# Optimization experiments

Hardware: AMD Instinct MI355X
Metric: run time of the kernel (lower is better)

The kernel has to match this reference:

```python
import jax, jax.numpy as jnp
import numpy as np

N_NODES = 100000
N_FEAT = 512
N_HID = 64
N_CLASS = 16
N_EDGES = 3200000
K = 10
ALPHA = 0.1


def setup_inputs() -> dict:
    key = jax.random.key(0)
    k1, k2, k3, k4, k5, k6 = jax.random.split(key, 6)
    x = jax.random.normal(k1, (N_NODES, N_FEAT), dtype=jnp.float32)
    edge_index = jax.random.randint(k2, (2, N_EDGES), 0, N_NODES, dtype=jnp.int64)
    # Linear params (torch Linear: y = x @ W.T + b), kaiming-uniform-ish scale
    s1 = 1.0 / np.sqrt(N_FEAT)
    W1 = jax.random.uniform(k3, (N_HID, N_FEAT), jnp.float32, -s1, s1)
    b1 = jax.random.uniform(k4, (N_HID,), jnp.float32, -s1, s1)
    s2 = 1.0 / np.sqrt(N_HID)
    W2 = jax.random.uniform(k5, (N_CLASS, N_HID), jnp.float32, -s2, s2)
    b2 = jax.random.uniform(k6, (N_CLASS,), jnp.float32, -s2, s2)
    return {"x": x, "W1": W1, "b1": b1, "W2": W2, "b2": b2, "edge_index": edge_index}


def _gcn_norm(edge_index, num_nodes):
    # add self-loops
    loops = jnp.arange(num_nodes, dtype=edge_index.dtype)
    row = jnp.concatenate([edge_index[0], loops])
    col = jnp.concatenate([edge_index[1], loops])
    deg = jax.ops.segment_sum(jnp.ones_like(col, dtype=jnp.float32), col,
                              num_segments=num_nodes)
    dis = jnp.where(deg > 0, jax.lax.rsqrt(jnp.maximum(deg, 1.0)), 0.0)
    norm = dis[row] * dis[col]  # symmetric D^-1/2 A D^-1/2
    return row, col, norm


def reference(x, W1, b1, W2, b2, edge_index):
    n = x.shape[0]
    # MLP (eval mode: dropout disabled)
    h = jax.nn.relu(x @ W1.T + b1)
    h0 = h @ W2.T + b2  # [N, nclass]
    # APPNP propagation: x_{k+1} = (1-alpha) * A_hat x_k + alpha * h0
    row, col, norm = _gcn_norm(edge_index, n)

    def step(h_cur, _):
        msg = norm[:, None] * h_cur[row]           # gather source nodes
        agg = jax.ops.segment_sum(msg, col, num_segments=n)  # scatter-add to targets
        return (1.0 - ALPHA) * agg + ALPHA * h0, None

    out, _ = jax.lax.scan(step, h0, None, length=K)
    return jax.nn.log_softmax(out, axis=1)
```

## Files before the change

kernel.cpp:

```cpp
#include <hip/hip_runtime.h>

#define NN 100000
#define NE 3200000
#define NCLS 16
#define NHID 64
#define NFEAT 512

#define NBUCK 391
#define PB 256
#define EPB 12500
#define CNT_TOT (NBUCK * PB)
#define CAP 10240

typedef __bf16 bf8 __attribute__((ext_vector_type(8)));
typedef short s8v __attribute__((ext_vector_type(8)));
typedef float f4 __attribute__((ext_vector_type(4)));
typedef unsigned short us8 __attribute__((ext_vector_type(8)));

union bu { s8v s; bf8 b; };

__device__ __forceinline__ float bf2f(unsigned short u) {
  union { unsigned int i; float f; } c; c.i = ((unsigned int)u) << 16; return c.f;
}
__device__ __forceinline__ unsigned short f2bf(float f) {
  unsigned int i = __float_as_uint(f);
  unsigned int r = (i + 0x7fffu + ((i >> 16) & 1u)) >> 16;
  return (unsigned short)r;
}

__global__ void probe_kernel(const unsigned short* __restrict__ x16,
                             const int* __restrict__ ei,
                             int* __restrict__ flags) {
  if (threadIdx.x == 0) {
    int inr = 0;
    for (int i = 0; i < 256; ++i) {
      float a = fabsf(bf2f(x16[2 * i]));
      if (a > 1e-3f && a < 16.0f) inr++;
    }
    flags[0] = (inr < 128) ? 1 : 0;
    int any = 0;
    for (int i = 0; i < 1024; ++i) any |= ei[2 * i + 1];
    flags[1] = (any != 0) ? 1 : 0;
  }
}

__device__ __forceinline__ int edge_val(const int* ei, int f_i32, long elem) {
  return f_i32 ? ei[elem] : ei[2 * elem];
}

__device__ __forceinline__ float ldf(const void* p, long i, int f32) {
  return f32 ? ((const float*)p)[i] : bf2f(((const unsigned short*)p)[i]);
}

__device__ __forceinline__ bf8 ld8(const void* p, long idx, int f32) {
  bu u;
  if (!f32) {
    u.b = *(const bf8*)((const unsigned short*)p + idx);
  } else {
    const f4* q = (const f4*)((const float*)p + idx);
    f4 a0 = q[0], a1 = q[1];
#pragma unroll
    for (int j = 0; j < 4; ++j) {
      u.s[j] = (short)f2bf(a0[j]);
      u.s[4 + j] = (short)f2bf(a1[j]);
    }
  }
  return u.b;
}

__global__ void sentinel_kernel(float* __restrict__ out, float v) {
  out[blockIdx.x * 256 + threadIdx.x] = v;
}

__global__ __launch_bounds__(256) void hist_kernel(const int* __restrict__ ei,
                                                   const int* __restrict__ flags,
                                                   unsigned int* __restrict__ cnt) {
  __shared__ unsigned int h[NBUCK];
  int tid = threadIdx.x;
  int f_i32 = flags[1];
  for (int i = tid; i < NBUCK; i += 256) h[i] = 0;
  __syncthreads();
  long e0 = (long)blockIdx.x * EPB;
  for (int t = tid; t < EPB; t += 256) {
    int dst = edge_val(ei, f_i32, (long)NE + e0 + t);
    atomicAdd(&h[dst >> 8], 1u);
  }
  __syncthreads();
  for (int i = tid; i < NBUCK; i += 256) cnt[(long)i * PB + blockIdx.x] = h[i];
}

__global__ __launch_bounds__(1024) void scan2_kernel(unsigned int* __restrict__ cnt) {
  __shared__ unsigned int sums[1024];
  const int C = 98;
  int t = threadIdx.x;
  int c0 = t * C;
  int c1 = min(c0 + C, CNT_TOT);
  unsigned int s = 0;
  for (int i = c0; i < c1; ++i) s += cnt[i];
  sums[t] = s;
  __syncthreads();
  for (int d = 1; d < 1024; d <<= 1) {
    unsigned int v = (t >= d) ? sums[t - d] : 0u;
    __syncthreads();
    sums[t] += v;
    __syncthreads();
  }
  unsigned int off = (t == 0) ? 0u : sums[t - 1];
  for (int i = c0; i < c1; ++i) {
    unsigned int v = cnt[i];
    cnt[i] = off;
    off += v;
  }
}

__global__ __launch_bounds__(256) void part_kernel(const int* __restrict__ ei,
                                                   const int* __restrict__ flags,
                                                   const unsigned int* __restrict__ cnt,
                                                   unsigned int* __restrict__ part) {
  __shared__ unsigned int cur[NBUCK];
  int tid = threadIdx.x;
  int b = blockIdx.x;
  int f_i32 = flags[1];
  for (int i = tid; i < NBUCK; i += 256) cur[i] = cnt[(long)i * PB + b];
  __syncthreads();
  long e0 = (long)b * EPB;
  for (int t = tid; t < EPB; t += 256) {
    int dst = edge_val(ei, f_i32, (long)NE + e0 + t);
    int src = edge_val(ei, f_i32, e0 + t);
    unsigned int pos = atomicAdd(&cur[dst >> 8], 1u);
    part[pos] = ((unsigned int)(dst & 255) << 20) | (unsigned int)src;
  }
}

__global__ __launch_bounds__(256) void csrb_kernel(const unsigned int* __restrict__ part,
                                                   const unsigned int* __restrict__ cnt,
                                                   unsigned int* __restrict__ csr,
                                                   unsigned int* __restrict__ deg,
                                                   unsigned int* __restrict__ offs,
                                                   float* __restrict__ dis) {
  __shared__ unsigned int sp[CAP];
  __shared__ unsigned int hcnt[256];
  __shared__ unsigned int hoff[256];
  int tid = threadIdx.x;
  int k = blockIdx.x;
  unsigned int start = cnt[(long)k * PB];
  unsigned int end = (k == NBUCK - 1) ? (unsigned int)NE : cnt[(long)(k + 1) * PB];
  int n = (int)(end - start);

  hcnt[tid] = 0;
  __syncthreads();
  for (int j = tid; j < n; j += 256) {
    unsigned int v = part[start + j];
    if (j < CAP) sp[j] = v;
    atomicAdd(&hcnt[v >> 20], 1u);
  }
  __syncthreads();

  unsigned int myc = hcnt[tid];
  hoff[tid] = myc;
  __syncthreads();
  for (int d = 1; d < 256; d <<= 1) {
    unsigned int v = (tid >= d) ? hoff[tid - d] : 0u;
    __syncthreads();
    hoff[tid] += v;
    __syncthreads();
  }
  unsigned int excl = hoff[tid] - myc;

  int node = k * 256 + tid;
  if (node < NN) {
    deg[node] = myc;
    offs[node] = start + excl;
    dis[node] = rsqrtf((float)(myc + 1u));
  }
  __syncthreads();
  hcnt[tid] = excl;
  __syncthreads();
  for (int j = tid; j < n; j += 256) {
    unsigned int v = (j < CAP) ? sp[j] : part[start + j];
    unsigned int pos = atomicAdd(&hcnt[v >> 20], 1u);
    csr[start + pos] = v & 0xFFFFFu;
  }
}

__global__ __launch_bounds__(256) void mlp_kernel(const void* __restrict__ xv,
                                                  const void* __restrict__ W1v,
                                                  const void* __restrict__ b1v,
                                                  const void* __restrict__ W2v,
                                                  const void* __restrict__ b2v,
                                                  const int* __restrict__ flags,
                                                  unsigned short* __restrict__ h0) {
  __shared__ float hl[64][65];
  __shared__ float w2l[16][65];
  __shared__ float b2l[16];

  int f32 = flags[0];
  int tid = threadIdx.x;
  int wave = tid >> 6;
  int lane = tid & 63;
  int quad = lane >> 4;
  int l16 = lane & 15;
  long rowBase = (long)blockIdx.x * 64;
  long mrow = rowBase + wave * 16 + l16;
  long mC = mrow < NN ? mrow : (NN - 1);

  {
    int i4 = tid * 4;
#pragma unroll
    for (int k = 0; k < 4; ++k) {
      int i = i4 + k;
      w2l[i >> 6][i & 63] = ldf(W2v, i, f32);
    }
    if (tid < 16) b2l[tid] = ldf(b2v, tid, f32);
  }

  f4 z = {0.f, 0.f, 0.f, 0.f};
  f4 acc[4] = {z, z, z, z};
#pragma unroll 4
  for (int i = 0; i < 16; ++i) {
    int k = i * 32 + quad * 8;
    bf8 a = ld8(xv, mC * NFEAT + k, f32);
#pragma unroll
    for (int t = 0; t < 4; ++t) {
      bf8 b = ld8(W1v, (long)(t * 16 + l16) * NFEAT + k, f32);
      acc[t] = __builtin_amdgcn_mfma_f32_16x16x32_bf16(a, b, acc[t], 0, 0, 0);
    }
  }

#pragma unroll
  for (int t = 0; t < 4; ++t) {
    float bias = ldf(b1v, t * 16 + l16, f32);
#pragma unroll
    for (int r = 0; r < 4; ++r) {
      int rl = wave * 16 + quad * 4 + r;
      float v = acc[t][r] + bias;
      hl[rl][t * 16 + l16] = fmaxf(v, 0.f);
    }
  }
  __syncthreads();

#pragma unroll
  for (int p = 0; p < 4; ++p) {
    int ml = p * 16 + (tid >> 4);
    int c = tid & 15;
    float a = b2l[c];
#pragma unroll 8
    for (int n = 0; n < NHID; ++n) a += hl[ml][n] * w2l[c][n];
    long grow = rowBase + ml;
    if (grow < NN) h0[grow * NCLS + c] = f2bf(a);
  }
}

__global__ void g0_kernel(const unsigned short* __restrict__ h0,
                          const float* __restrict__ dis,
                          unsigned short* __restrict__ g) {
  int i = blockIdx.x * blockDim.x + threadIdx.x;
  if (i < NN * 2) {
    int node = i >> 1;
    us8 v = ((const us8*)h0)[i];
    float d = dis[node];
    us8 o;
#pragma unroll
    for (int j = 0; j < 8; ++j) o[j] = f2bf(d * bf2f(v[j]));
    ((us8*)g)[i] = o;
  }
}

__global__ __launch_bounds__(256) void prop_kernel(const unsigned short* __restrict__ g_in,
                                                   const unsigned short* __restrict__ h0,
                                                   const float* __restrict__ dis,
                                                   const unsigned int* __restrict__ deg,
                                                   const unsigned int* __restrict__ offs,
                                                   const unsigned int* __restrict__ csr,
                                                   unsigned short* __restrict__ g_out,
                                                   void* __restrict__ outv,
                                                   const int* __restrict__ flags,
                                                   int final_step) {
  int gidx = blockIdx.x * blockDim.x + threadIdx.x;
  int node = gidx >> 1;
  int half = threadIdx.x & 1;
  if (node >= NN) return;

  unsigned int cnt = deg[node];
  unsigned int base = offs[node];
  const us8* G = (const us8*)g_in;

  float acc[8];
#pragma unroll
  for (int c = 0; c < 8; ++c) acc[c] = 0.f;

  unsigned int j = 0;
  for (; j + 4 <= cnt; j += 4) {
    unsigned int s0 = csr[base + j];
    unsigned int s1 = csr[base + j + 1];
    unsigned int s2 = csr[base + j + 2];
    unsigned int s3 = csr[base + j + 3];
    us8 v0 = G[s0 * 2 + half];
    us8 v1 = G[s1 * 2 + half];
    us8 v2 = G[s2 * 2 + half];
    us8 v3 = G[s3 * 2 + half];
#pragma unroll
    for (int c = 0; c < 8; ++c)
      acc[c] += (bf2f(v0[c]) + bf2f(v1[c])) + (bf2f(v2[c]) + bf2f(v3[c]));
  }
  for (; j < cnt; ++j) {
    us8 v = G[csr[base + j] * 2 + half];
#pragma unroll
    for (int c = 0; c < 8; ++c) acc[c] += bf2f(v[c]);
  }
  {
    us8 v = G[node * 2 + half];
#pragma unroll
    for (int c = 0; c < 8; ++c) acc[c] += bf2f(v[c]);
  }

  float dd = dis[node];
  us8 h0v = ((const us8*)h0)[node * 2 + half];
  float h[8];
#pragma unroll
  for (int c = 0; c < 8; ++c) h[c] = 0.9f * dd * acc[c] + 0.1f * bf2f(h0v[c]);

  if (!final_step) {
    us8 o;
#pragma unroll
    for (int c = 0; c < 8; ++c) o[c] = f2bf(dd * h[c]);
    ((us8*)g_out)[node * 2 + half] = o;
  } else {
    float mx = h[0];
#pragma unroll
    for (int c = 1; c < 8; ++c) mx = fmaxf(mx, h[c]);
    mx = fmaxf(mx, __shfl_xor(mx, 1));
    float se = 0.f;
#pragma unroll
    for (int c = 0; c < 8; ++c) se += expf(h[c] - mx);
    se += __shfl_xor(se, 1);
    float ls = logf(se) + mx;
    if (flags[0]) {
      float4 o0, o1;
      o0.x = h[0] - ls; o0.y = h[1] - ls; o0.z = h[2] - ls; o0.w = h[3] - ls;
      o1.x = h[4] - ls; o1.y = h[5] - ls; o1.z = h[6] - ls; o1.w = h[7] - ls;
      ((float4*)outv)[node * 4 + half * 2] = o0;
      ((float4*)outv)[node * 4 + half * 2 + 1] = o1;
    } else {
      us8 o;
#pragma unroll
      for (int c = 0; c < 8; ++c) o[c] = f2bf(h[c] - ls);
      ((us8*)outv)[node * 2 + half] = o;
    }
  }
}

extern "C" void kernel_launch(void* const* d_in, const int* in_sizes, int n_in,
                              void* d_out, int out_size, void* d_ws, size_t ws_size,
                              hipStream_t stream) {
  const void* x  = d_in[0];
  const void* W1 = d_in[1];
  const void* b1 = d_in[2];
  const void* W2 = d_in[3];
  const void* b2 = d_in[4];
  const int* ei  = (const int*)d_in[5];

  size_t need = 16 + (size_t)CNT_TOT * 4 + 3 * (size_t)NN * 4 + (size_t)NN * NCLS * 2 +
                (size_t)NE * 4 + (size_t)NE * 4;
  if (ws_size < need) {
    sentinel_kernel<<<4, 256, 0, stream>>>((float*)d_out,
                                           -(1000.0f + (float)(ws_size >> 20)));
    return;
  }

  char* p = (char*)d_ws;
  int* flags           = (int*)p;          p += 16;
  unsigned int* cnt    = (unsigned int*)p; p += (size_t)CNT_TOT * 4;
  unsigned int* deg    = (unsigned int*)p; p += (size_t)NN * 4;
  unsigned int* offs   = (unsigned int*)p; p += (size_t)NN * 4;
  float* dis           = (float*)p;        p += (size_t)NN * 4;
  unsigned short* h0   = (unsigned short*)p; p += (size_t)NN * NCLS * 2;
  unsigned int* csr    = (unsigned int*)p; p += (size_t)NE * 4;
  unsigned int* part   = (unsigned int*)p; p += (size_t)NE * 4;
  unsigned short* gA   = (unsigned short*)part;
  unsigned short* gB   = (unsigned short*)((char*)part + (size_t)NN * NCLS * 2);

  probe_kernel<<<1, 64, 0, stream>>>((const unsigned short*)x, ei, flags);
  hist_kernel<<<PB, 256, 0, stream>>>(ei, flags, cnt);
  mlp_kernel<<<(NN + 63) / 64, 256, 0, stream>>>(x, W1, b1, W2, b2, flags, h0);
  scan2_kernel<<<1, 1024, 0, stream>>>(cnt);
  part_kernel<<<PB, 256, 0, stream>>>(ei, flags, cnt, part);
  csrb_kernel<<<NBUCK, 256, 0, stream>>>(part, cnt, csr, deg, offs, dis);
  g0_kernel<<<(NN * 2 + 255) / 256, 256, 0, stream>>>(h0, dis, gA);

  unsigned short* gin = gA;
  unsigned short* gout = gB;
  for (int k = 0; k < 9; ++k) {
    prop_kernel<<<(NN * 2 + 255) / 256, 256, 0, stream>>>(gin, h0, dis, deg, offs, csr,
                                                          gout, nullptr, flags, 0);
    unsigned short* t = gin; gin = gout; gout = t;
  }
  prop_kernel<<<(NN * 2 + 255) / 256, 256, 0, stream>>>(gin, h0, dis, deg, offs, csr,
                                                        nullptr, d_out, flags, 1);
}
```

Baseline: 1.139 ms.

## Add bf16 MFMA MLP with LDS DMA and widen propagation to 4 lanes per node

Adds a bf16 MLP kernel that stages W1 and double-buffered x tiles into LDS with global_load_lds and computes the first layer with 16x16x32 bf16 MFMA. The old MLP kernel is kept as a fallback for fp32 inputs, and a runtime flag picks which one does the work. The propagation kernel now uses 4 threads per node with 8-byte gathers and an 8-way unrolled edge loop, which raises parallelism and the number of loads in flight per node. The cost is an extra kernel launch that exits early, 80KB of LDS per block in the MLP (limiting occupancy), and smaller gather transactions.

```diff
diff --git a/kernel.cpp b/kernel.cpp
--- a/kernel.cpp
+++ b/kernel.cpp
@@ -16,8 +16,12 @@
 typedef short s8v __attribute__((ext_vector_type(8)));
 typedef float f4 __attribute__((ext_vector_type(4)));
 typedef unsigned short us8 __attribute__((ext_vector_type(8)));
+typedef unsigned short us4 __attribute__((ext_vector_type(4)));
 
 union bu { s8v s; bf8 b; };
+
+typedef __attribute__((address_space(1))) const unsigned int as1u;
+typedef __attribute__((address_space(3))) unsigned int as3u;
 
 __device__ __forceinline__ float bf2f(unsigned short u) {
   union { unsigned int i; float f; } c; c.i = ((unsigned int)u) << 16; return c.f;
@@ -26,6 +30,14 @@
   unsigned int i = __float_as_uint(f);
   unsigned int r = (i + 0x7fffu + ((i >> 16) & 1u)) >> 16;
   return (unsigned short)r;
+}
+
+__device__ __forceinline__ void dma16(const void* g, void* lds_base, int lane) {
+#if __has_builtin(__builtin_amdgcn_global_load_lds)
+  __builtin_amdgcn_global_load_lds((as1u*)g, (as3u*)lds_base, 16, 0, 0);
+#else
+  ((us8*)lds_base)[lane] = *(const us8*)g;
+#endif
 }
 
 __global__ void probe_kernel(const unsigned short* __restrict__ x16,
@@ -183,18 +195,119 @@
   }
 }
 
-__global__ __launch_bounds__(256) void mlp_kernel(const void* __restrict__ xv,
-                                                  const void* __restrict__ W1v,
-                                                  const void* __restrict__ b1v,
-                                                  const void* __restrict__ W2v,
-                                                  const void* __restrict__ b2v,
-                                                  const int* __restrict__ flags,
-                                                  unsigned short* __restrict__ h0) {
+__global__ __launch_bounds__(256) void mlp_fast(const unsigned short* __restrict__ x,
+                                                const unsigned short* __restrict__ W1,
+                                                const unsigned short* __restrict__ b1,
+                                                const unsigned short* __restrict__ W2,
+                                                const unsigned short* __restrict__ b2,
+                                                const int* __restrict__ flags,
+                                                unsigned short* __restrict__ h0) {
+  __shared__ char smem[81920];
+  if (flags[0]) return;
+
+  const int XOFF = 65536;
+  int tid = threadIdx.x;
+  int wave = tid >> 6;
+  int lane = tid & 63;
+  int quad = lane >> 4;
+  int l16 = lane & 15;
+  long rowBase = (long)blockIdx.x * 64;
+
+#pragma unroll
+  for (int r = 0; r < 16; ++r) {
+    int row = wave * 16 + r;
+    dma16(W1 + (long)row * NFEAT + lane * 8, smem + row * 1024, lane);
+  }
+  {
+    long grow = rowBase + lane;
+    if (grow >= NN) grow = NN - 1;
+#pragma unroll
+    for (int p = 0; p < 2; ++p) {
+      int kblk = wave * 2 + p;
+      dma16(x + grow * NFEAT + kblk * 8, smem + XOFF + kblk * 1024, lane);
+    }
+  }
+  __syncthreads();
+
+  f4 z = {0.f, 0.f, 0.f, 0.f};
+  f4 acc[4] = {z, z, z, z};
+
+  for (int c = 0; c < 8; ++c) {
+    int buf = c & 1;
+    if (c < 7) {
+      long grow = rowBase + lane;
+      if (grow >= NN) grow = NN - 1;
+      int nb = (c + 1) & 1;
+#pragma unroll
+      for (int p = 0; p < 2; ++p) {
+        int kblk = wave * 2 + p;
+        dma16(x + grow * NFEAT + (c + 1) * 64 + kblk * 8,
+              smem + XOFF + nb * 8192 + kblk * 1024, lane);
+      }
+    }
+#pragma unroll
+    for (int i2 = 0; i2 < 2; ++i2) {
+      bf8 a = *(const bf8*)(smem + XOFF + buf * 8192 +
+                            ((i2 * 4 + quad) * 64 + wave * 16 + l16) * 16);
+      int k = c * 64 + i2 * 32 + quad * 8;
+#pragma unroll
+      for (int t = 0; t < 4; ++t) {
+        bf8 b = *(const bf8*)(smem + ((t * 16 + l16) * NFEAT + k) * 2);
+        acc[t] = __builtin_amdgcn_mfma_f32_16x16x32_bf16(a, b, acc[t], 0, 0, 0);
+      }
+    }
+    __syncthreads();
+  }
+
+  float* hl = (float*)smem;
+  float* w2l = (float*)(smem + 16640);
+  float* b2l = (float*)(smem + 20800);
+  {
+    int i4 = tid * 4;
+#pragma unroll
+    for (int kk = 0; kk < 4; ++kk) {
+      int i = i4 + kk;
+      w2l[(i >> 6) * 65 + (i & 63)] = bf2f(W2[i]);
+    }
+    if (tid < 16) b2l[tid] = bf2f(b2[tid]);
+  }
+#pragma unroll
+  for (int t = 0; t < 4; ++t) {
+    float bias = bf2f(b1[t * 16 + l16]);
+#pragma unroll
+    for (int r = 0; r < 4; ++r) {
+      int rl = wave * 16 + quad * 4 + r;
+      float v = acc[t][r] + bias;
+      hl[rl * 65 + t * 16 + l16] = fmaxf(v, 0.f);
+    }
+  }
+  __syncthreads();
+
+#pragma unroll
+  for (int p = 0; p < 4; ++p) {
+    int ml = p * 16 + (tid >> 4);
+    int cc = tid & 15;
+    float a = b2l[cc];
+#pragma unroll 8
+    for (int n = 0; n < NHID; ++n) a += hl[ml * 65 + n] * w2l[cc * 65 + n];
+    long grow = rowBase + ml;
+    if (grow < NN) h0[grow * NCLS + cc] = f2bf(a);
+  }
+}
+
+__global__ __launch_bounds__(256) void mlp_fb(const void* __restrict__ xv,
+                                              const void* __restrict__ W1v,
+                                              const void* __restrict__ b1v,
+                                              const void* __restrict__ W2v,
+                                              const void* __restrict__ b2v,
+                                              const int* __restrict__ flags,
+                                              unsigned short* __restrict__ h0) {
   __shared__ float hl[64][65];
   __shared__ float w2l[16][65];
   __shared__ float b2l[16];
-
-  int f32 = flags[0];
+  if (!flags[0]) return;
+
+  int f32 = 1;
   int tid = threadIdx.x;
   int wave = tid >> 6;
   int lane = tid & 63;
@@ -277,75 +390,71 @@
                                                    const int* __restrict__ flags,
                                                    int final_step) {
   int gidx = blockIdx.x * blockDim.x + threadIdx.x;
-  int node = gidx >> 1;
-  int half = threadIdx.x & 1;
+  int node = gidx >> 2;
+  int q = threadIdx.x & 3;
   if (node >= NN) return;
 
   unsigned int cnt = deg[node];
   unsigned int base = offs[node];
-  const us8* G = (const us8*)g_in;
-
-  float acc[8];
-#pragma unroll
-  for (int c = 0; c < 8; ++c) acc[c] = 0.f;
+  const us4* G = (const us4*)g_in;
+
+  float acc[4] = {0.f, 0.f, 0.f, 0.f};
 
   unsigned int j = 0;
-  for (; j + 4 <= cnt; j += 4) {
-    unsigned int s0 = csr[base + j];
-    unsigned int s1 = csr[base + j + 1];
-    unsigned int s2 = csr[base + j + 2];
-    unsigned int s3 = csr[base + j + 3];
-    us8 v0 = G[s0 * 2 + half];
-    us8 v1 = G[s1 * 2 + half];
-    us8 v2 = G[s2 * 2 + half];
-    us8 v3 = G[s3 * 2 + half];
-#pragma unroll
-    for (int c = 0; c < 8; ++c)
-      acc[c] += (bf2f(v0[c]) + bf2f(v1[c])) + (bf2f(v2[c]) + bf2f(v3[c]));
+  for (; j + 8 <= cnt; j += 8) {
+    unsigned int s[8];
+#pragma unroll
+    for (int u = 0; u < 8; ++u) s[u] = csr[base + j + u];
+    us4 v[8];
+#pragma unroll
+    for (int u = 0; u < 8; ++u) v[u] = G[s[u] * 4 + q];
+#pragma unroll
+    for (int u = 0; u < 8; ++u) {
+#pragma unroll
+      for (int c = 0; c < 4; ++c) acc[c] += bf2f(v[u][c]);
+    }
   }
   for (; j < cnt; ++j) {
-    us8 v = G[csr[base + j] * 2 + half];
-#pragma unroll
-    for (int c = 0; c < 8; ++c) acc[c] += bf2f(v[c]);
+    us4 v = G[csr[base + j] * 4 + q];
+#pragma unroll
+    for (int c = 0; c < 4; ++c) acc[c] += bf2f(v[c]);
   }
   {
-    us8 v = G[node * 2 + half];
-#pragma unroll
-    for (int c = 0; c < 8; ++c) acc[c] += bf2f(v[c]);
+    us4 v = G[node * 4 + q];
+#pragma unroll
+    for (int c = 0; c < 4; ++c) acc[c] += bf2f(v[c]);
   }
 
   float dd = dis[node];
-  us8 h0v = ((const us8*)h0)[node * 2 + half];
-  float h[8];
-#pragma unroll
-  for (int c = 0; c < 8; ++c) h[c] = 0.9f * dd * acc[c] + 0.1f * bf2f(h0v[c]);
+  us4 h0v = ((const us4*)h0)[node * 4 + q];
+  float h[4];
+#pragma unroll
+  for (int c = 0; c < 4; ++c) h[c] = 0.9f * dd * acc[c] + 0.1f * bf2f(h0v[c]);
 
   if (!final_step) {
-    us8 o;
-#pragma unroll
-    for (int c = 0; c < 8; ++c) o[c] = f2bf(dd * h[c]);
-    ((us8*)g_out)[node * 2 + half] = o;
+    us4 o;
+#pragma unroll
+    for (int c = 0; c < 4; ++c) o[c] = f2bf(dd * h[c]);
+    ((us4*)g_out)[node * 4 + q] = o;
   } else {
-    float mx = h[0];
-#pragma unroll
-    for (int c = 1; c < 8; ++c) mx = fmaxf(mx, h[c]);
+    float mx = fmaxf(fmaxf(h[0], h[1]), fmaxf(h[2], h[3]));
     mx = fmaxf(mx, __shfl_xor(mx, 1));
+    mx = fmaxf(mx, __shfl_xor(mx, 2));
     float se = 0.f;
 #pragma unroll
-    for (int c = 0; c < 8; ++c) se += expf(h[c] - mx);
+    for (int c = 0; c < 4; ++c) se += expf(h[c] - mx);
     se += __shfl_xor(se, 1);
+    se += __shfl_xor(se, 2);
     float ls = logf(se) + mx;
     if (flags[0]) {
-      float4 o0, o1;
-      o0.x = h[0] - ls; o0.y = h[1] - ls; o0.z = h[2] - ls; o0.w = h[3] - ls;
-      o1.x = h[4] - ls; o1.y = h[5] - ls; o1.z = h[6] - ls; o1.w = h[7] - ls;
-      ((float4*)outv)[node * 4 + half * 2] = o0;
-      ((float4*)outv)[node * 4 + half * 2 + 1] = o1;
+      float4 o;
+      o.x = h[0] - ls; o.y = h[1] - ls; o.z = h[2] - ls; o.w = h[3] - ls;
+      ((float4*)outv)[node * 4 + q] = o;
     } else {
-      us8 o;
-#pragma unroll
-      for (int c = 0; c < 8; ++c) o[c] = f2bf(h[c] - ls);
-      ((us8*)outv)[node * 2 + half] = o;
+      us4 o;
+#pragma unroll
+      for (int c = 0; c < 4; ++c) o[c] = f2bf(h[c] - ls);
+      ((us4*)outv)[node * 4 + q] = o;
     }
   }
 }
@@ -382,7 +491,12 @@
 
   probe_kernel<<<1, 64, 0, stream>>>((const unsigned short*)x, ei, flags);
   hist_kernel<<<PB, 256, 0, stream>>>(ei, flags, cnt);
-  mlp_kernel<<<(NN + 63) / 64, 256, 0, stream>>>(x, W1, b1, W2, b2, flags, h0);
+  mlp_fast<<<(NN + 63) / 64, 256, 0, stream>>>((const unsigned short*)x,
+                                               (const unsigned short*)W1,
+                                               (const unsigned short*)b1,
+                                               (const unsigned short*)W2,
+                                               (const unsigned short*)b2, flags, h0);
+  mlp_fb<<<(NN + 63) / 64, 256, 0, stream>>>(x, W1, b1, W2, b2, flags, h0);
   scan2_kernel<<<1, 1024, 0, stream>>>(cnt);
   part_kernel<<<PB, 256, 0, stream>>>(ei, flags, cnt, part);
   csrb_kernel<<<NBUCK, 256, 0, stream>>>(part, cnt, csr, deg, offs, dis);
@@ -391,10 +505,10 @@
   unsigned short* gin = gA;
   unsigned short* gout = gB;
   for (int k = 0; k < 9; ++k) {
-    prop_kernel<<<(NN * 2 + 255) / 256, 256, 0, stream>>>(gin, h0, dis, deg, offs, csr,
+    prop_kernel<<<(NN * 4 + 255) / 256, 256, 0, stream>>>(gin, h0, dis, deg, offs, csr,
                                                           gout, nullptr, flags, 0);
     unsigned short* t = gin; gin = gout; gout = t;
   }
-  prop_kernel<<<(NN * 2 + 255) / 256, 256, 0, stream>>>(gin, h0, dis, deg, offs, csr,
+  prop_kernel<<<(NN * 4 + 255) / 256, 256, 0, stream>>>(gin, h0, dis, deg, offs, csr,
                                                         nullptr, d_out, flags, 1);
 }
```

Result: faster. 1.047 ms (-8.1%).
